# Kernel tuning notes

Measured on AMD Instinct MI355X. Metric: run time of the kernel, lower is better.

## Reference

```python
import jax, jax.numpy as jnp
import numpy as np


def _lstm_layer(x_sbi, w_ih, w_hh, b):
    """Custom LSTM layer with elu candidate/cell activations.
    x_sbi: [S, B, I]; w_ih: [4H, I]; w_hh: [4H, H]; b: [4H]. Gate order i,f,g,o.
    Returns outputs [S, B, H].
    """
    H = w_hh.shape[1]
    S, B, _ = x_sbi.shape
    # Precompute the input projection for all timesteps at once.
    xw = jnp.einsum('sbi,gi->sbg', x_sbi, w_ih) + b  # [S, B, 4H]

    def step(carry, xt):
        h, c = carry
        gates = xt + h @ w_hh.T  # [B, 4H]
        i = jax.nn.sigmoid(gates[:, 0 * H:1 * H])
        f = jax.nn.sigmoid(gates[:, 1 * H:2 * H])
        g = jax.nn.elu(gates[:, 2 * H:3 * H])      # custom cell activation
        o = jax.nn.sigmoid(gates[:, 3 * H:4 * H])
        c = f * c + i * g
        h = o * jax.nn.elu(c)                       # custom hidden activation
        return (h, c), h

    h0 = jnp.zeros((B, H), dtype=x_sbi.dtype)
    c0 = jnp.zeros((B, H), dtype=x_sbi.dtype)
    _, out = jax.lax.scan(step, (h0, c0), xw)
    return out  # [S, B, H]


def setup_inputs() -> dict:
    key = jax.random.key(0)
    ks = jax.random.split(key, 12)
    B, S, I, H = 256, 512, 64, 512
    s_in = 1.0 / np.sqrt(H)
    d = {
        'x': jax.random.normal(ks[0], (B, S, I), dtype=jnp.float32),
        'w_ih1': jax.random.normal(ks[1], (4 * H, I), dtype=jnp.float32) * s_in,
        'w_hh1': jax.random.normal(ks[2], (4 * H, H), dtype=jnp.float32) * s_in,
        'b1': jax.random.normal(ks[3], (4 * H,), dtype=jnp.float32) * s_in,
        'w_ih2': jax.random.normal(ks[4], (4 * H, H), dtype=jnp.float32) * s_in,
        'w_hh2': jax.random.normal(ks[5], (4 * H, H), dtype=jnp.float32) * s_in,
        'b2': jax.random.normal(ks[6], (4 * H,), dtype=jnp.float32) * s_in,
        'w_ih3': jax.random.normal(ks[7], (4 * H, H), dtype=jnp.float32) * s_in,
        'w_hh3': jax.random.normal(ks[8], (4 * H, H), dtype=jnp.float32) * s_in,
        'b3': jax.random.normal(ks[9], (4 * H,), dtype=jnp.float32) * s_in,
        'fc_w': jax.random.normal(ks[10], (1, H), dtype=jnp.float32) * s_in,
        'fc_b': jax.random.normal(ks[11], (1,), dtype=jnp.float32) * s_in,
    }
    return d


def reference(x, w_ih1, w_hh1, b1, w_ih2, w_hh2, b2, w_ih3, w_hh3, b3, fc_w, fc_b):
    # x: [B, S, I] -> seq-first [S, B, I] (matches torch permute(1,0,2))
    out = jnp.transpose(x, (1, 0, 2))
    out = _lstm_layer(out, w_ih1, w_hh1, b1)  # dropout = identity (eval)
    out = _lstm_layer(out, w_ih2, w_hh2, b2)
    out = _lstm_layer(out, w_ih3, w_hh3, b3)
    last = out[-1]                             # [B, H]
    return last @ fc_w.T + fc_b                # [B, 1]
```

## Files before the change

### kernel.cpp

```cpp
#include <hip/hip_runtime.h>
#include <stdint.h>
#include <stddef.h>

#define S_LEN 512
#define BATCH 256
#define NIN   64
#define HD    512
#define G4    2048
#define RING_D 32
#define BT    64

typedef _Float16 f16;
typedef _Float16 f16x8 __attribute__((ext_vector_type(8)));
typedef float    f32x4 __attribute__((ext_vector_type(4)));
typedef uint32_t u32x4 __attribute__((ext_vector_type(4)));
typedef uint64_t u64x2 __attribute__((ext_vector_type(2)));

__global__ void k_f32_to_f16(const float* __restrict__ src, f16* __restrict__ dst, int n) {
  int i = blockIdx.x * 256 + threadIdx.x;
  if (i < n) dst[i] = (f16)src[i];
}

__global__ void k_x_transpose(const float* __restrict__ x, f16* __restrict__ xin) {
  int idx = blockIdx.x * 256 + threadIdx.x;
  int i  = idx & 63;
  int sb = idx >> 6;
  int b  = sb & 255;
  int s  = sb >> 8;
  xin[idx] = (f16)x[((size_t)b * S_LEN + s) * NIN + i];
}

__global__ void k_zero_i32(uint32_t* p, int n) {
  int i = blockIdx.x * 256 + threadIdx.x;
  if (i < n) p[i] = 0u;
}

__global__ __launch_bounds__(512, 2) void k_fused(
    const f16* __restrict__ whh,
    const f16* __restrict__ wih,
    const float* __restrict__ b0,
    const float* __restrict__ b1,
    const float* __restrict__ b2,
    const f16* __restrict__ xin,
    f16* __restrict__ ring,
    int* __restrict__ flags,
    f16* __restrict__ hlast) {
  const int tid  = threadIdx.x;
  const int lane = tid & 63;
  const int wave = tid >> 6;
  const int l    = blockIdx.x >> 6;
  const int bi   = (blockIdx.x >> 4) & 3;
  const int gi   = blockIdx.x & 15;
  const int ln   = lane & 15;
  const int quad = lane >> 4;
  const int g    = wave >> 1;
  const int kh   = wave & 1;

  __shared__ __align__(16) char smem[131072];
  char*  lh_b  = smem;
  char*  lhp_b = smem + 65536;
  float* lg0   = (float*)smem;
  float* lg1   = (float*)(smem + 32768);

  auto swz = [](int row, int boff) { return row * 1024 + (boff ^ ((row & 7) << 4)); };

  const f16* whh_l = whh + (size_t)l * G4 * HD;
  const f16* wih_l = wih + (size_t)l * G4 * HD;
  const float* bias_l = (l == 0) ? b0 : (l == 1 ? b1 : b2);

  f16x8 wf[16][2];
  if (kh == 0 || l > 0) {
    const f16* W = kh ? wih_l : whh_l;
#pragma unroll
    for (int nb = 0; nb < 2; nb++) {
      const int r = g * 512 + gi * 32 + nb * 16 + ln;
#pragma unroll
      for (int ks = 0; ks < 16; ks++) {
        u32x4 tmp = *(const u32x4*)(W + (size_t)r * HD + ks * 32 + quad * 8);
        asm volatile("" : "+v"(tmp));
        wf[ks][nb] = __builtin_bit_cast(f16x8, tmp);
      }
    }
  } else {
#pragma unroll
    for (int nb = 0; nb < 2; nb++) {
      const int r = g * 512 + gi * 32 + nb * 16 + ln;
#pragma unroll
      for (int ks = 0; ks < 2; ks++) {
        u32x4 tmp = *(const u32x4*)(wih_l + (size_t)r * NIN + ks * 32 + quad * 8);
        asm volatile("" : "+v"(tmp));
        wf[ks][nb] = __builtin_bit_cast(f16x8, tmp);
      }
    }
  }

  const int brow = tid >> 5;
  const int hl_  = tid & 31;
  float cv[4] = {0.f, 0.f, 0.f, 0.f};
  const float bv0 = bias_l[0 * HD + gi * 32 + hl_];
  const float bv1 = bias_l[1 * HD + gi * 32 + hl_];
  const float bv2 = bias_l[2 * HD + gi * 32 + hl_];
  const float bv3 = bias_l[3 * HD + gi * 32 + hl_];

  int* fown = flags + l * 64 + bi * 16;
  int* myflag = fown + gi;
  const int* fprev = (l > 0) ? (flags + (l - 1) * 64 + bi * 16) : fown;
  const int* fnext = (l < 2) ? (flags + (l + 1) * 64 + bi * 16) : fown;

  for (int t = 0; t < S_LEN; t++) {
    {
      const int* fp = fown;
      int need = t;
      if (quad == 1 && l > 0)      { fp = fprev; need = t + 1; }
      else if (quad == 2 && l < 2) { fp = fnext; need = t + 2 - RING_D; }
      int v = __hip_atomic_load(fp + ln, __ATOMIC_RELAXED, __HIP_MEMORY_SCOPE_AGENT);
      while (!__all(v >= need)) {
        __builtin_amdgcn_s_sleep(1);
        v = __hip_atomic_load(fp + ln, __ATOMIC_RELAXED, __HIP_MEMORY_SCOPE_AGENT);
      }
    }
    asm volatile("" ::: "memory");

    const uint64_t* hown = (const uint64_t*)(ring
        + ((size_t)l * RING_D + (t & (RING_D - 1))) * (BATCH * HD)
        + (size_t)(bi * BT) * HD);
    uint64_t a0[8], a1[8];
#pragma unroll
    for (int j = 0; j < 8; j++) {
      a0[j] = __hip_atomic_load(hown + j * 1024 + tid * 2,     __ATOMIC_RELAXED, __HIP_MEMORY_SCOPE_AGENT);
      a1[j] = __hip_atomic_load(hown + j * 1024 + tid * 2 + 1, __ATOMIC_RELAXED, __HIP_MEMORY_SCOPE_AGENT);
    }
    if (l > 0) {
      const uint64_t* hprev = (const uint64_t*)(ring
          + ((size_t)(l - 1) * RING_D + ((t + 1) & (RING_D - 1))) * (BATCH * HD)
          + (size_t)(bi * BT) * HD);
      uint64_t p0[8], p1[8];
#pragma unroll
      for (int j = 0; j < 8; j++) {
        p0[j] = __hip_atomic_load(hprev + j * 1024 + tid * 2,     __ATOMIC_RELAXED, __HIP_MEMORY_SCOPE_AGENT);
        p1[j] = __hip_atomic_load(hprev + j * 1024 + tid * 2 + 1, __ATOMIC_RELAXED, __HIP_MEMORY_SCOPE_AGENT);
      }
#pragma unroll
      for (int j = 0; j < 8; j++) {
        const int e = j * 1024 + tid * 2, row = e >> 7, c8 = e & 127;
        u64x2 p; p[0] = p0[j]; p[1] = p1[j];
        *(u64x2*)(lhp_b + swz(row, c8 * 8)) = p;
      }
    } else {
      const int xr = tid >> 3, xc = tid & 7;
      u32x4 xv = *(const u32x4*)(xin + ((size_t)(t * 256 + bi * BT + xr)) * NIN + xc * 8);
      *(u32x4*)(lhp_b + swz(xr, xc * 16)) = xv;
    }
#pragma unroll
    for (int j = 0; j < 8; j++) {
      const int e = j * 1024 + tid * 2, row = e >> 7, c8 = e & 127;
      u64x2 p; p[0] = a0[j]; p[1] = a1[j];
      *(u64x2*)(lh_b + swz(row, c8 * 8)) = p;
    }
    __syncthreads();

    f32x4 acc[4][2] = {};
    const char* tb = kh ? lhp_b : lh_b;
    if (kh == 0 || l > 0) {
#pragma unroll
      for (int ks = 0; ks < 16; ks++) {
        f16x8 af[4];
#pragma unroll
        for (int mi = 0; mi < 4; mi++)
          af[mi] = *(const f16x8*)(tb + swz(mi * 16 + ln, ks * 64 + quad * 16));
#pragma unroll
        for (int mi = 0; mi < 4; mi++)
#pragma unroll
          for (int nb = 0; nb < 2; nb++)
            acc[mi][nb] = __builtin_amdgcn_mfma_f32_16x16x32_f16(af[mi], wf[ks][nb], acc[mi][nb], 0, 0, 0);
      }
    } else {
#pragma unroll
      for (int ks = 0; ks < 2; ks++) {
        f16x8 af[4];
#pragma unroll
        for (int mi = 0; mi < 4; mi++)
          af[mi] = *(const f16x8*)(tb + swz(mi * 16 + ln, ks * 64 + quad * 16));
#pragma unroll
        for (int mi = 0; mi < 4; mi++)
#pragma unroll
          for (int nb = 0; nb < 2; nb++)
            acc[mi][nb] = __builtin_amdgcn_mfma_f32_16x16x32_f16(af[mi], wf[ks][nb], acc[mi][nb], 0, 0, 0);
      }
    }
    __syncthreads();

    {
      float* lg = kh ? lg1 : lg0;
#pragma unroll
      for (int mi = 0; mi < 4; mi++)
#pragma unroll
        for (int nb = 0; nb < 2; nb++)
#pragma unroll
          for (int rr = 0; rr < 4; rr++) {
            const int row = mi * 16 + quad * 4 + rr;
            const int col = g * 32 + nb * 16 + ln;
            lg[row * 128 + (col ^ (((row >> 2) & 7) << 2))] = acc[mi][nb][rr];
          }
    }
    __syncthreads();

    f16* hout = ring + ((size_t)l * RING_D + ((t + 1) & (RING_D - 1))) * (BATCH * HD);
#pragma unroll
    for (int s = 0; s < 4; s++) {
      const int row = brow + s * 16;
      const int xm = ((row >> 2) & 7) << 2;
      const int rb = row * 128;
      float g0 = lg0[rb + ((0  + hl_) ^ xm)] + lg1[rb + ((0  + hl_) ^ xm)] + bv0;
      float g1 = lg0[rb + ((32 + hl_) ^ xm)] + lg1[rb + ((32 + hl_) ^ xm)] + bv1;
      float g2 = lg0[rb + ((64 + hl_) ^ xm)] + lg1[rb + ((64 + hl_) ^ xm)] + bv2;
      float g3 = lg0[rb + ((96 + hl_) ^ xm)] + lg1[rb + ((96 + hl_) ^ xm)] + bv3;
      const float igt = 1.f / (1.f + __expf(-g0));
      const float fgt = 1.f / (1.f + __expf(-g1));
      const float ggt = g2 > 0.f ? g2 : expm1f(g2);
      const float ogt = 1.f / (1.f + __expf(-g3));
      cv[s] = fgt * cv[s] + igt * ggt;
      const float hv = ogt * (cv[s] > 0.f ? cv[s] : expm1f(cv[s]));
      f16 hv16 = (f16)hv;
      unsigned short us;
      __builtin_memcpy(&us, &hv16, 2);
      const size_t col = (size_t)(bi * BT + row) * HD + gi * 32 + hl_;
      __hip_atomic_store((unsigned short*)(hout + col), us,
                         __ATOMIC_RELAXED, __HIP_MEMORY_SCOPE_AGENT);
      if (l == 2 && t == S_LEN - 1) hlast[col] = hv16;
    }
    __syncthreads();
    if (tid == 0)
      __hip_atomic_store(myflag, t + 1, __ATOMIC_RELAXED, __HIP_MEMORY_SCOPE_AGENT);
  }
}

__global__ __launch_bounds__(64) void k_fc(const f16* __restrict__ hlast,
                                           const float* __restrict__ fcw,
                                           const float* __restrict__ fcb,
                                           float* __restrict__ out) {
  const int b = blockIdx.x, lane = threadIdx.x;
  const f16* hp = hlast + (size_t)b * HD + lane * 8;
  float s = 0.f;
#pragma unroll
  for (int j = 0; j < 8; j++) s += (float)hp[j] * fcw[lane * 8 + j];
  for (int off = 32; off; off >>= 1) s += __shfl_down(s, off);
  if (lane == 0) out[b] = s + fcb[0];
}

extern "C" void kernel_launch(void* const* d_in, const int* in_sizes, int n_in,
                              void* d_out, int out_size, void* d_ws, size_t ws_size,
                              hipStream_t stream) {
  (void)in_sizes; (void)n_in; (void)out_size; (void)ws_size;
  const float* x      = (const float*)d_in[0];
  const float* wih[3] = {(const float*)d_in[1], (const float*)d_in[4], (const float*)d_in[7]};
  const float* whh[3] = {(const float*)d_in[2], (const float*)d_in[5], (const float*)d_in[8]};
  const float* bia[3] = {(const float*)d_in[3], (const float*)d_in[6], (const float*)d_in[9]};
  const float* fcw = (const float*)d_in[10];
  const float* fcb = (const float*)d_in[11];
  float* out = (float*)d_out;

  char* ws = (char*)d_ws;
  size_t off = 0;
  auto alloc = [&](size_t bytes) -> char* {
    off = (off + 255) & ~(size_t)255;
    char* p = ws + off;
    off += bytes;
    return p;
  };

  f16* xin   = (f16*)alloc((size_t)S_LEN * BATCH * NIN * 2);
  f16* wih16 = (f16*)alloc((size_t)3 * G4 * HD * 2);
  f16* whh16 = (f16*)alloc((size_t)3 * G4 * HD * 2);
  f16* ring  = (f16*)alloc((size_t)3 * RING_D * BATCH * HD * 2);
  int* flags = (int*)alloc(256 * 4);
  f16* hlast = (f16*)alloc((size_t)BATCH * HD * 2);

  {
    int n = S_LEN * BATCH * NIN;
    k_x_transpose<<<dim3(n / 256), dim3(256), 0, stream>>>(x, xin);
  }
  k_f32_to_f16<<<dim3((G4 * NIN + 255) / 256), dim3(256), 0, stream>>>(wih[0], wih16, G4 * NIN);
  k_f32_to_f16<<<dim3((G4 * HD + 255) / 256), dim3(256), 0, stream>>>(wih[1], wih16 + (size_t)G4 * HD, G4 * HD);
  k_f32_to_f16<<<dim3((G4 * HD + 255) / 256), dim3(256), 0, stream>>>(wih[2], wih16 + (size_t)2 * G4 * HD, G4 * HD);
  for (int l = 0; l < 3; l++)
    k_f32_to_f16<<<dim3((G4 * HD + 255) / 256), dim3(256), 0, stream>>>(whh[l], whh16 + (size_t)l * G4 * HD, G4 * HD);
  for (int l = 0; l < 3; l++)
    k_zero_i32<<<dim3(BATCH * HD / 2 / 256), dim3(256), 0, stream>>>(
        (uint32_t*)(ring + (size_t)l * RING_D * BATCH * HD), BATCH * HD / 2);
  k_zero_i32<<<dim3(1), dim3(256), 0, stream>>>((uint32_t*)flags, 192);

  k_fused<<<dim3(192), dim3(512), 0, stream>>>(whh16, wih16, bia[0], bia[1], bia[2],
                                               xin, ring, flags, hlast);

  k_fc<<<dim3(BATCH), dim3(64), 0, stream>>>(hlast, fcw, fcb, out);
}
```

Measured before the change: 5.788 ms.

## Overlap input-projection MFMA and next-step prefetch with recurrent h loads

Splits waves by role. The input-side waves (kh=1) compute the input/previous-layer projection into a shared gate buffer while the recurrent-side waves (kh=0) wait for and load h_{t-1}. Afterwards the kh=0 waves run the recurrent MFMA and accumulate into that buffer, while the kh=1 waves prefetch the next timestep's input (x or the lower layer's h). This takes the input projection and its loads off the critical recurrent path and replaces the double gate buffer with a single summed one. It also swaps expm1f for __expf-1, which is cheaper but loses some accuracy near zero, and raises LDS use to 160KB.

```diff
diff --git a/kernel.cpp b/kernel.cpp
--- a/kernel.cpp
+++ b/kernel.cpp
@@ -55,14 +55,15 @@
   const int quad = lane >> 4;
   const int g    = wave >> 1;
   const int kh   = wave & 1;
-
-  __shared__ __align__(16) char smem[131072];
+  const int gt   = (wave >> 1) * 64 + lane;
+
+  __shared__ __align__(16) char smem[163840];
   char*  lh_b  = smem;
   char*  lhp_b = smem + 65536;
-  float* lg0   = (float*)smem;
-  float* lg1   = (float*)(smem + 32768);
+  float* lgsum = (float*)(smem + 131072);
 
   auto swz = [](int row, int boff) { return row * 1024 + (boff ^ ((row & 7) << 4)); };
+  auto lgpos = [](int row, int col) { return row * 128 + (col ^ (((row >> 2) & 7) << 2)); };
 
   const f16* whh_l = whh + (size_t)l * G4 * HD;
   const f16* wih_l = wih + (size_t)l * G4 * HD;
@@ -107,91 +108,81 @@
   const int* fprev = (l > 0) ? (flags + (l - 1) * 64 + bi * 16) : fown;
   const int* fnext = (l < 2) ? (flags + (l + 1) * 64 + bi * 16) : fown;
 
-  for (int t = 0; t < S_LEN; t++) {
-    {
-      const int* fp = fown;
-      int need = t;
-      if (quad == 1 && l > 0)      { fp = fprev; need = t + 1; }
-      else if (quad == 2 && l < 2) { fp = fnext; need = t + 2 - RING_D; }
-      int v = __hip_atomic_load(fp + ln, __ATOMIC_RELAXED, __HIP_MEMORY_SCOPE_AGENT);
-      while (!__all(v >= need)) {
-        __builtin_amdgcn_s_sleep(1);
-        v = __hip_atomic_load(fp + ln, __ATOMIC_RELAXED, __HIP_MEMORY_SCOPE_AGENT);
-      }
+  if (l > 0) {
+    int v = __hip_atomic_load(fprev + ln, __ATOMIC_RELAXED, __HIP_MEMORY_SCOPE_AGENT);
+    while (!__all(v >= 1)) {
+      __builtin_amdgcn_s_sleep(1);
+      v = __hip_atomic_load(fprev + ln, __ATOMIC_RELAXED, __HIP_MEMORY_SCOPE_AGENT);
     }
     asm volatile("" ::: "memory");
-
-    const uint64_t* hown = (const uint64_t*)(ring
-        + ((size_t)l * RING_D + (t & (RING_D - 1))) * (BATCH * HD)
-        + (size_t)(bi * BT) * HD);
-    uint64_t a0[8], a1[8];
+    const uint64_t* hp = (const uint64_t*)(ring
+        + ((size_t)(l - 1) * RING_D + 1) * (BATCH * HD) + (size_t)(bi * BT) * HD);
+    uint64_t p0[8], p1[8];
 #pragma unroll
     for (int j = 0; j < 8; j++) {
-      a0[j] = __hip_atomic_load(hown + j * 1024 + tid * 2,     __ATOMIC_RELAXED, __HIP_MEMORY_SCOPE_AGENT);
-      a1[j] = __hip_atomic_load(hown + j * 1024 + tid * 2 + 1, __ATOMIC_RELAXED, __HIP_MEMORY_SCOPE_AGENT);
-    }
-    if (l > 0) {
-      const uint64_t* hprev = (const uint64_t*)(ring
-          + ((size_t)(l - 1) * RING_D + ((t + 1) & (RING_D - 1))) * (BATCH * HD)
-          + (size_t)(bi * BT) * HD);
-      uint64_t p0[8], p1[8];
-#pragma unroll
-      for (int j = 0; j < 8; j++) {
-        p0[j] = __hip_atomic_load(hprev + j * 1024 + tid * 2,     __ATOMIC_RELAXED, __HIP_MEMORY_SCOPE_AGENT);
-        p1[j] = __hip_atomic_load(hprev + j * 1024 + tid * 2 + 1, __ATOMIC_RELAXED, __HIP_MEMORY_SCOPE_AGENT);
-      }
-#pragma unroll
-      for (int j = 0; j < 8; j++) {
-        const int e = j * 1024 + tid * 2, row = e >> 7, c8 = e & 127;
-        u64x2 p; p[0] = p0[j]; p[1] = p1[j];
-        *(u64x2*)(lhp_b + swz(row, c8 * 8)) = p;
-      }
-    } else {
-      const int xr = tid >> 3, xc = tid & 7;
-      u32x4 xv = *(const u32x4*)(xin + ((size_t)(t * 256 + bi * BT + xr)) * NIN + xc * 8);
-      *(u32x4*)(lhp_b + swz(xr, xc * 16)) = xv;
+      p0[j] = __hip_atomic_load(hp + j * 1024 + tid * 2,     __ATOMIC_RELAXED, __HIP_MEMORY_SCOPE_AGENT);
+      p1[j] = __hip_atomic_load(hp + j * 1024 + tid * 2 + 1, __ATOMIC_RELAXED, __HIP_MEMORY_SCOPE_AGENT);
     }
 #pragma unroll
     for (int j = 0; j < 8; j++) {
       const int e = j * 1024 + tid * 2, row = e >> 7, c8 = e & 127;
-      u64x2 p; p[0] = a0[j]; p[1] = a1[j];
-      *(u64x2*)(lh_b + swz(row, c8 * 8)) = p;
-    }
-    __syncthreads();
-
-    f32x4 acc[4][2] = {};
-    const char* tb = kh ? lhp_b : lh_b;
-    if (kh == 0 || l > 0) {
-#pragma unroll
-      for (int ks = 0; ks < 16; ks++) {
+      u64x2 p; p[0] = p0[j]; p[1] = p1[j];
+      *(u64x2*)(lhp_b + swz(row, c8 * 8)) = p;
+    }
+  } else {
+    const int xr = tid >> 3, xc = tid & 7;
+    u32x4 xv = *(const u32x4*)(xin + ((size_t)(bi * BT + xr)) * NIN + xc * 8);
+    *(u32x4*)(lhp_b + swz(xr, xc * 16)) = xv;
+  }
+  __syncthreads();
+
+  for (int t = 0; t < S_LEN; t++) {
+    const bool lastT = (t == S_LEN - 1);
+
+    if (kh == 0) {
+      {
+        const int* fp = fown; int need = t;
+        if (quad == 2 && l < 2) { fp = fnext; need = t - 28; }
+        int v = __hip_atomic_load(fp + ln, __ATOMIC_RELAXED, __HIP_MEMORY_SCOPE_AGENT);
+        while (!__all(v >= need)) {
+          __builtin_amdgcn_s_sleep(1);
+          v = __hip_atomic_load(fp + ln, __ATOMIC_RELAXED, __HIP_MEMORY_SCOPE_AGENT);
+        }
+      }
+      asm volatile("" ::: "memory");
+      const uint64_t* hown = (const uint64_t*)(ring
+          + ((size_t)l * RING_D + (t & (RING_D - 1))) * (BATCH * HD)
+          + (size_t)(bi * BT) * HD);
+#pragma unroll
+      for (int b = 0; b < 2; b++) {
+        uint64_t q0[8], q1[8];
+#pragma unroll
+        for (int j = 0; j < 8; j++) {
+          const int e = (b * 8 + j) * 512 + gt * 2;
+          q0[j] = __hip_atomic_load(hown + e,     __ATOMIC_RELAXED, __HIP_MEMORY_SCOPE_AGENT);
+          q1[j] = __hip_atomic_load(hown + e + 1, __ATOMIC_RELAXED, __HIP_MEMORY_SCOPE_AGENT);
+        }
+#pragma unroll
+        for (int j = 0; j < 8; j++) {
+          const int e = (b * 8 + j) * 512 + gt * 2, row = e >> 7, c8 = e & 127;
+          u64x2 p; p[0] = q0[j]; p[1] = q1[j];
+          *(u64x2*)(lh_b + swz(row, c8 * 8)) = p;
+        }
+      }
+    } else {
+      f32x4 acc[4][2] = {};
+      const int nks = (l == 0) ? 2 : 16;
+      for (int ks = 0; ks < nks; ks++) {
         f16x8 af[4];
 #pragma unroll
         for (int mi = 0; mi < 4; mi++)
-          af[mi] = *(const f16x8*)(tb + swz(mi * 16 + ln, ks * 64 + quad * 16));
+          af[mi] = *(const f16x8*)(lhp_b + swz(mi * 16 + ln, ks * 64 + quad * 16));
 #pragma unroll
         for (int mi = 0; mi < 4; mi++)
 #pragma unroll
           for (int nb = 0; nb < 2; nb++)
             acc[mi][nb] = __builtin_amdgcn_mfma_f32_16x16x32_f16(af[mi], wf[ks][nb], acc[mi][nb], 0, 0, 0);
       }
-    } else {
-#pragma unroll
-      for (int ks = 0; ks < 2; ks++) {
-        f16x8 af[4];
-#pragma unroll
-        for (int mi = 0; mi < 4; mi++)
-          af[mi] = *(const f16x8*)(tb + swz(mi * 16 + ln, ks * 64 + quad * 16));
-#pragma unroll
-        for (int mi = 0; mi < 4; mi++)
-#pragma unroll
-          for (int nb = 0; nb < 2; nb++)
-            acc[mi][nb] = __builtin_amdgcn_mfma_f32_16x16x32_f16(af[mi], wf[ks][nb], acc[mi][nb], 0, 0, 0);
-      }
-    }
-    __syncthreads();
-
-    {
-      float* lg = kh ? lg1 : lg0;
 #pragma unroll
       for (int mi = 0; mi < 4; mi++)
 #pragma unroll
@@ -200,8 +191,70 @@
           for (int rr = 0; rr < 4; rr++) {
             const int row = mi * 16 + quad * 4 + rr;
             const int col = g * 32 + nb * 16 + ln;
-            lg[row * 128 + (col ^ (((row >> 2) & 7) << 2))] = acc[mi][nb][rr];
+            lgsum[lgpos(row, col)] = acc[mi][nb][rr];
           }
+    }
+    __syncthreads();
+
+    if (kh == 0) {
+      f32x4 acc[4][2] = {};
+#pragma unroll
+      for (int ks = 0; ks < 16; ks++) {
+        f16x8 af[4];
+#pragma unroll
+        for (int mi = 0; mi < 4; mi++)
+          af[mi] = *(const f16x8*)(lh_b + swz(mi * 16 + ln, ks * 64 + quad * 16));
+#pragma unroll
+        for (int mi = 0; mi < 4; mi++)
+#pragma unroll
+          for (int nb = 0; nb < 2; nb++)
+            acc[mi][nb] = __builtin_amdgcn_mfma_f32_16x16x32_f16(af[mi], wf[ks][nb], acc[mi][nb], 0, 0, 0);
+      }
+#pragma unroll
+      for (int mi = 0; mi < 4; mi++)
+#pragma unroll
+        for (int nb = 0; nb < 2; nb++)
+#pragma unroll
+          for (int rr = 0; rr < 4; rr++) {
+            const int row = mi * 16 + quad * 4 + rr;
+            const int col = g * 32 + nb * 16 + ln;
+            lgsum[lgpos(row, col)] += acc[mi][nb][rr];
+          }
+    } else if (!lastT) {
+      if (l > 0) {
+        int v = __hip_atomic_load(fprev + ln, __ATOMIC_RELAXED, __HIP_MEMORY_SCOPE_AGENT);
+        while (!__all(v >= t + 2)) {
+          __builtin_amdgcn_s_sleep(1);
+          v = __hip_atomic_load(fprev + ln, __ATOMIC_RELAXED, __HIP_MEMORY_SCOPE_AGENT);
+        }
+        asm volatile("" ::: "memory");
+        const uint64_t* hp = (const uint64_t*)(ring
+            + ((size_t)(l - 1) * RING_D + ((t + 2) & (RING_D - 1))) * (BATCH * HD)
+            + (size_t)(bi * BT) * HD);
+#pragma unroll
+        for (int b = 0; b < 2; b++) {
+          uint64_t q0[8], q1[8];
+#pragma unroll
+          for (int j = 0; j < 8; j++) {
+            const int e = (b * 8 + j) * 512 + gt * 2;
+            q0[j] = __hip_atomic_load(hp + e,     __ATOMIC_RELAXED, __HIP_MEMORY_SCOPE_AGENT);
+            q1[j] = __hip_atomic_load(hp + e + 1, __ATOMIC_RELAXED, __HIP_MEMORY_SCOPE_AGENT);
+          }
+#pragma unroll
+          for (int j = 0; j < 8; j++) {
+            const int e = (b * 8 + j) * 512 + gt * 2, row = e >> 7, c8 = e & 127;
+            u64x2 p; p[0] = q0[j]; p[1] = q1[j];
+            *(u64x2*)(lhp_b + swz(row, c8 * 8)) = p;
+          }
+        }
+      } else {
+#pragma unroll
+        for (int j = 0; j < 2; j++) {
+          const int cid = j * 256 + gt, xr = cid >> 3, xc = cid & 7;
+          u32x4 xv = *(const u32x4*)(xin + ((size_t)((t + 1) * 256 + bi * BT + xr)) * NIN + xc * 8);
+          *(u32x4*)(lhp_b + swz(xr, xc * 16)) = xv;
+        }
+      }
     }
     __syncthreads();
 
@@ -209,18 +262,16 @@
 #pragma unroll
     for (int s = 0; s < 4; s++) {
       const int row = brow + s * 16;
-      const int xm = ((row >> 2) & 7) << 2;
-      const int rb = row * 128;
-      float g0 = lg0[rb + ((0  + hl_) ^ xm)] + lg1[rb + ((0  + hl_) ^ xm)] + bv0;
-      float g1 = lg0[rb + ((32 + hl_) ^ xm)] + lg1[rb + ((32 + hl_) ^ xm)] + bv1;
-      float g2 = lg0[rb + ((64 + hl_) ^ xm)] + lg1[rb + ((64 + hl_) ^ xm)] + bv2;
-      float g3 = lg0[rb + ((96 + hl_) ^ xm)] + lg1[rb + ((96 + hl_) ^ xm)] + bv3;
+      float g0 = lgsum[lgpos(row, 0  + hl_)] + bv0;
+      float g1 = lgsum[lgpos(row, 32 + hl_)] + bv1;
+      float g2 = lgsum[lgpos(row, 64 + hl_)] + bv2;
+      float g3 = lgsum[lgpos(row, 96 + hl_)] + bv3;
       const float igt = 1.f / (1.f + __expf(-g0));
       const float fgt = 1.f / (1.f + __expf(-g1));
-      const float ggt = g2 > 0.f ? g2 : expm1f(g2);
+      const float ggt = g2 > 0.f ? g2 : (__expf(g2) - 1.f);
       const float ogt = 1.f / (1.f + __expf(-g3));
       cv[s] = fgt * cv[s] + igt * ggt;
-      const float hv = ogt * (cv[s] > 0.f ? cv[s] : expm1f(cv[s]));
+      const float hv = ogt * (cv[s] > 0.f ? cv[s] : (__expf(cv[s]) - 1.f));
       f16 hv16 = (f16)hv;
       unsigned short us;
       __builtin_memcpy(&us, &hv16, 2);
```

New measurement: 9.875 ms. 70.6% more time.

## Prefetch previous-layer input via direct global-to-LDS loads and overlap with gate math

Applied to the files above, without the earlier changes.

Replaces the register-staged atomic loads of the recurrent and previous-layer hidden states with global_load_lds DMA straight into swizzled LDS. The previous-layer or x input for step t+1 is now fetched at the end of step t, after the gate epilogue, so its latency is moved off the start of the next step. The loop also collapses the two MFMA branches into one with a variable trip count, swaps expm1f for __expf-1, and drops a full __syncthreads in favour of a raw s_barrier. This risks memory-ordering subtleties: plain DMA loads replace agent-scope atomics, the LDS slot reuse now relies on the waitcnt and barrier placement, and __expf-1 loses precision near zero.

```diff
diff --git a/kernel.cpp b/kernel.cpp
--- a/kernel.cpp
+++ b/kernel.cpp
@@ -14,7 +14,13 @@
 typedef _Float16 f16x8 __attribute__((ext_vector_type(8)));
 typedef float    f32x4 __attribute__((ext_vector_type(4)));
 typedef uint32_t u32x4 __attribute__((ext_vector_type(4)));
-typedef uint64_t u64x2 __attribute__((ext_vector_type(2)));
+
+typedef __attribute__((address_space(3))) void lds_as;
+typedef const __attribute__((address_space(1))) void glb_as;
+
+static __device__ __forceinline__ void gll16(const void* g, void* l) {
+  __builtin_amdgcn_global_load_lds((glb_as*)g, (lds_as*)l, 16, 0, 17);
+}
 
 __global__ void k_f32_to_f16(const float* __restrict__ src, f16* __restrict__ dst, int n) {
   int i = blockIdx.x * 256 + threadIdx.x;
@@ -63,6 +69,7 @@
   float* lg1   = (float*)(smem + 32768);
 
   auto swz = [](int row, int boff) { return row * 1024 + (boff ^ ((row & 7) << 4)); };
+  auto lgpos = [](int row, int col) { return row * 128 + (col ^ (((row >> 2) & 7) << 2)); };
 
   const f16* whh_l = whh + (size_t)l * G4 * HD;
   const f16* wih_l = wih + (size_t)l * G4 * HD;
@@ -107,12 +114,31 @@
   const int* fprev = (l > 0) ? (flags + (l - 1) * 64 + bi * 16) : fown;
   const int* fnext = (l < 2) ? (flags + (l + 1) * 64 + bi * 16) : fown;
 
+  if (l > 0) {
+    int v = __hip_atomic_load(fprev + ln, __ATOMIC_RELAXED, __HIP_MEMORY_SCOPE_AGENT);
+    while (!__all(v >= 1)) {
+      __builtin_amdgcn_s_sleep(1);
+      v = __hip_atomic_load(fprev + ln, __ATOMIC_RELAXED, __HIP_MEMORY_SCOPE_AGENT);
+    }
+    asm volatile("" ::: "memory");
+    const f16* src = ring + ((size_t)(l - 1) * RING_D + 1) * (BATCH * HD)
+                   + (size_t)(bi * BT) * HD;
+#pragma unroll
+    for (int jj = 0; jj < 8; jj++) {
+      const int r = wave * 8 + jj;
+      const int gb = (lane * 16) ^ ((r & 7) << 4);
+      gll16((const char*)(src + (size_t)r * HD) + gb, lhp_b + r * 1024);
+    }
+  } else {
+    const int xr = tid >> 3, xc = tid & 7;
+    u32x4 xv = *(const u32x4*)(xin + ((size_t)(bi * BT + xr)) * NIN + xc * 8);
+    *(u32x4*)(lhp_b + swz(xr, xc * 16)) = xv;
+  }
+
   for (int t = 0; t < S_LEN; t++) {
     {
-      const int* fp = fown;
-      int need = t;
-      if (quad == 1 && l > 0)      { fp = fprev; need = t + 1; }
-      else if (quad == 2 && l < 2) { fp = fnext; need = t + 2 - RING_D; }
+      const int* fp = fown; int need = t;
+      if (quad == 2 && l < 2) { fp = fnext; need = t - 28; }
       int v = __hip_atomic_load(fp + ln, __ATOMIC_RELAXED, __HIP_MEMORY_SCOPE_AGENT);
       while (!__all(v >= need)) {
         __builtin_amdgcn_s_sleep(1);
@@ -121,72 +147,36 @@
     }
     asm volatile("" ::: "memory");
 
-    const uint64_t* hown = (const uint64_t*)(ring
-        + ((size_t)l * RING_D + (t & (RING_D - 1))) * (BATCH * HD)
-        + (size_t)(bi * BT) * HD);
-    uint64_t a0[8], a1[8];
-#pragma unroll
-    for (int j = 0; j < 8; j++) {
-      a0[j] = __hip_atomic_load(hown + j * 1024 + tid * 2,     __ATOMIC_RELAXED, __HIP_MEMORY_SCOPE_AGENT);
-      a1[j] = __hip_atomic_load(hown + j * 1024 + tid * 2 + 1, __ATOMIC_RELAXED, __HIP_MEMORY_SCOPE_AGENT);
-    }
-    if (l > 0) {
-      const uint64_t* hprev = (const uint64_t*)(ring
-          + ((size_t)(l - 1) * RING_D + ((t + 1) & (RING_D - 1))) * (BATCH * HD)
-          + (size_t)(bi * BT) * HD);
-      uint64_t p0[8], p1[8];
-#pragma unroll
-      for (int j = 0; j < 8; j++) {
-        p0[j] = __hip_atomic_load(hprev + j * 1024 + tid * 2,     __ATOMIC_RELAXED, __HIP_MEMORY_SCOPE_AGENT);
-        p1[j] = __hip_atomic_load(hprev + j * 1024 + tid * 2 + 1, __ATOMIC_RELAXED, __HIP_MEMORY_SCOPE_AGENT);
-      }
-#pragma unroll
-      for (int j = 0; j < 8; j++) {
-        const int e = j * 1024 + tid * 2, row = e >> 7, c8 = e & 127;
-        u64x2 p; p[0] = p0[j]; p[1] = p1[j];
-        *(u64x2*)(lhp_b + swz(row, c8 * 8)) = p;
-      }
-    } else {
+    {
+      const f16* src = ring + ((size_t)l * RING_D + (t & (RING_D - 1))) * (BATCH * HD)
+                     + (size_t)(bi * BT) * HD;
+#pragma unroll
+      for (int jj = 0; jj < 8; jj++) {
+        const int r = wave * 8 + jj;
+        const int gb = (lane * 16) ^ ((r & 7) << 4);
+        gll16((const char*)(src + (size_t)r * HD) + gb, lh_b + r * 1024);
+      }
+    }
+    u32x4 xv = {};
+    if (l == 0 && t + 1 < S_LEN) {
       const int xr = tid >> 3, xc = tid & 7;
-      u32x4 xv = *(const u32x4*)(xin + ((size_t)(t * 256 + bi * BT + xr)) * NIN + xc * 8);
-      *(u32x4*)(lhp_b + swz(xr, xc * 16)) = xv;
-    }
-#pragma unroll
-    for (int j = 0; j < 8; j++) {
-      const int e = j * 1024 + tid * 2, row = e >> 7, c8 = e & 127;
-      u64x2 p; p[0] = a0[j]; p[1] = a1[j];
-      *(u64x2*)(lh_b + swz(row, c8 * 8)) = p;
+      xv = *(const u32x4*)(xin + ((size_t)((t + 1) * 256 + bi * BT + xr)) * NIN + xc * 8);
     }
     __syncthreads();
 
     f32x4 acc[4][2] = {};
     const char* tb = kh ? lhp_b : lh_b;
-    if (kh == 0 || l > 0) {
-#pragma unroll
-      for (int ks = 0; ks < 16; ks++) {
-        f16x8 af[4];
-#pragma unroll
-        for (int mi = 0; mi < 4; mi++)
-          af[mi] = *(const f16x8*)(tb + swz(mi * 16 + ln, ks * 64 + quad * 16));
-#pragma unroll
-        for (int mi = 0; mi < 4; mi++)
-#pragma unroll
-          for (int nb = 0; nb < 2; nb++)
-            acc[mi][nb] = __builtin_amdgcn_mfma_f32_16x16x32_f16(af[mi], wf[ks][nb], acc[mi][nb], 0, 0, 0);
-      }
-    } else {
-#pragma unroll
-      for (int ks = 0; ks < 2; ks++) {
-        f16x8 af[4];
-#pragma unroll
-        for (int mi = 0; mi < 4; mi++)
-          af[mi] = *(const f16x8*)(tb + swz(mi * 16 + ln, ks * 64 + quad * 16));
-#pragma unroll
-        for (int mi = 0; mi < 4; mi++)
-#pragma unroll
-          for (int nb = 0; nb < 2; nb++)
-            acc[mi][nb] = __builtin_amdgcn_mfma_f32_16x16x32_f16(af[mi], wf[ks][nb], acc[mi][nb], 0, 0, 0);
-      }
+    const int nks = (kh && l == 0) ? 2 : 16;
+    for (int ks = 0; ks < nks; ks++) {
+      f16x8 af[4];
+#pragma unroll
+      for (int mi = 0; mi < 4; mi++)
+        af[mi] = *(const f16x8*)(tb + swz(mi * 16 + ln, ks * 64 + quad * 16));
+#pragma unroll
+      for (int mi = 0; mi < 4; mi++)
+#pragma unroll
+        for (int nb = 0; nb < 2; nb++)
+          acc[mi][nb] = __builtin_amdgcn_mfma_f32_16x16x32_f16(af[mi], wf[ks][nb], acc[mi][nb], 0, 0, 0);
     }
     __syncthreads();
 
@@ -217,10 +207,10 @@
       float g3 = lg0[rb + ((96 + hl_) ^ xm)] + lg1[rb + ((96 + hl_) ^ xm)] + bv3;
       const float igt = 1.f / (1.f + __expf(-g0));
       const float fgt = 1.f / (1.f + __expf(-g1));
-      const float ggt = g2 > 0.f ? g2 : expm1f(g2);
+      const float ggt = g2 > 0.f ? g2 : (__expf(g2) - 1.f);
       const float ogt = 1.f / (1.f + __expf(-g3));
       cv[s] = fgt * cv[s] + igt * ggt;
-      const float hv = ogt * (cv[s] > 0.f ? cv[s] : expm1f(cv[s]));
+      const float hv = ogt * (cv[s] > 0.f ? cv[s] : (__expf(cv[s]) - 1.f));
       f16 hv16 = (f16)hv;
       unsigned short us;
       __builtin_memcpy(&us, &hv16, 2);
@@ -229,7 +219,33 @@
                          __ATOMIC_RELAXED, __HIP_MEMORY_SCOPE_AGENT);
       if (l == 2 && t == S_LEN - 1) hlast[col] = hv16;
     }
-    __syncthreads();
+
+    asm volatile("s_waitcnt vmcnt(0)" ::: "memory");
+
+    if (t + 1 < S_LEN) {
+      if (l > 0) {
+        int v = __hip_atomic_load(fprev + ln, __ATOMIC_RELAXED, __HIP_MEMORY_SCOPE_AGENT);
+        while (!__all(v >= t + 2)) {
+          __builtin_amdgcn_s_sleep(1);
+          v = __hip_atomic_load(fprev + ln, __ATOMIC_RELAXED, __HIP_MEMORY_SCOPE_AGENT);
+        }
+        asm volatile("" ::: "memory");
+        const f16* src = ring + ((size_t)(l - 1) * RING_D + ((t + 2) & (RING_D - 1))) * (BATCH * HD)
+                       + (size_t)(bi * BT) * HD;
+#pragma unroll
+        for (int jj = 0; jj < 8; jj++) {
+          const int r = wave * 8 + jj;
+          const int gb = (lane * 16) ^ ((r & 7) << 4);
+          gll16((const char*)(src + (size_t)r * HD) + gb, lhp_b + r * 1024);
+        }
+      } else {
+        const int xr = tid >> 3, xc = tid & 7;
+        *(u32x4*)(lhp_b + swz(xr, xc * 16)) = xv;
+      }
+    }
+
+    __builtin_amdgcn_s_barrier();
+    __builtin_amdgcn_sched_barrier(0);
     if (tid == 0)
       __hip_atomic_store(myflag, t + 1, __ATOMIC_RELAXED, __HIP_MEMORY_SCOPE_AGENT);
   }
```

New measurement: 7.721 ms. 33.4% more time.

## Map LSTM blocks to XCDs and read same-XCD recurrent state through L2 with direct LDS loads

Applied to the files above, without the earlier changes.

Blocks are remapped so that layers 0-1 of each batch slice share one XCD and layer 2 sits on its own XCD. At startup each block records its hardware XCC id and checks whether its producers share it. When they do, the hidden state is read from a second, non-atomic ring copy using global_load_lds straight into LDS, so the L2 is used instead of device-scope atomic loads. The ring depth also shrinks from 32 to 8, and expm1f is replaced by __expf-1. In exchange every step writes two copies of the state, the launch adds 64 idle blocks, and coherence between the two ring copies rests on the assumed XCD placement.

```diff
diff --git a/kernel.cpp b/kernel.cpp
--- a/kernel.cpp
+++ b/kernel.cpp
@@ -7,7 +7,7 @@
 #define NIN   64
 #define HD    512
 #define G4    2048
-#define RING_D 32
+#define RING_D 8
 #define BT    64
 
 typedef _Float16 f16;
@@ -15,6 +15,13 @@
 typedef float    f32x4 __attribute__((ext_vector_type(4)));
 typedef uint32_t u32x4 __attribute__((ext_vector_type(4)));
 typedef uint64_t u64x2 __attribute__((ext_vector_type(2)));
+
+typedef __attribute__((address_space(3))) void lds_as;
+typedef const __attribute__((address_space(1))) void glb_as;
+
+static __device__ __forceinline__ void gll16_l2(const void* g, void* l) {
+  __builtin_amdgcn_global_load_lds((glb_as*)g, (lds_as*)l, 16, 0, 1);
+}
 
 __global__ void k_f32_to_f16(const float* __restrict__ src, f16* __restrict__ dst, int n) {
   int i = blockIdx.x * 256 + threadIdx.x;
@@ -42,15 +49,19 @@
     const float* __restrict__ b1,
     const float* __restrict__ b2,
     const f16* __restrict__ xin,
-    f16* __restrict__ ring,
+    f16* __restrict__ ringM,
+    f16* __restrict__ ringL,
     int* __restrict__ flags,
+    int* __restrict__ xcdmap,
     f16* __restrict__ hlast) {
   const int tid  = threadIdx.x;
   const int lane = tid & 63;
   const int wave = tid >> 6;
-  const int l    = blockIdx.x >> 6;
-  const int bi   = (blockIdx.x >> 4) & 3;
-  const int gi   = blockIdx.x & 15;
+  const int xcd  = blockIdx.x & 7;
+  const int slot = blockIdx.x >> 3;
+  int l, bi, gi;
+  if (xcd < 4) { bi = xcd; l = slot >> 4; gi = slot & 15; }
+  else         { if (slot >= 16) return; l = 2; bi = xcd - 4; gi = slot; }
   const int ln   = lane & 15;
   const int quad = lane >> 4;
   const int g    = wave >> 1;
@@ -63,10 +74,37 @@
   float* lg1   = (float*)(smem + 32768);
 
   auto swz = [](int row, int boff) { return row * 1024 + (boff ^ ((row & 7) << 4)); };
+  auto bid_of = [](int ll, int bb, int gg) {
+    return (ll == 2) ? ((gg << 3) | (bb + 4)) : ((((ll << 4) + gg) << 3) | bb);
+  };
 
   const f16* whh_l = whh + (size_t)l * G4 * HD;
   const f16* wih_l = wih + (size_t)l * G4 * HD;
   const float* bias_l = (l == 0) ? b0 : (l == 1 ? b1 : b2);
+
+  unsigned myxcc;
+  asm volatile("s_getreg_b32 %0, hwreg(HW_REG_XCC_ID)" : "=s"(myxcc));
+  if (tid == 0)
+    __hip_atomic_store(xcdmap + blockIdx.x, (int)myxcc + 1, __ATOMIC_RELAXED, __HIP_MEMORY_SCOPE_AGENT);
+  bool lh_local = false, lhp_local = false;
+  {
+    const int mb = bid_of(l, bi, ln);
+    int v = __hip_atomic_load(xcdmap + mb, __ATOMIC_RELAXED, __HIP_MEMORY_SCOPE_AGENT);
+    while (!__all(v > 0)) {
+      __builtin_amdgcn_s_sleep(2);
+      v = __hip_atomic_load(xcdmap + mb, __ATOMIC_RELAXED, __HIP_MEMORY_SCOPE_AGENT);
+    }
+    lh_local = __all(v == (int)myxcc + 1);
+  }
+  if (l == 1) {
+    const int pb = bid_of(0, bi, ln);
+    int v = __hip_atomic_load(xcdmap + pb, __ATOMIC_RELAXED, __HIP_MEMORY_SCOPE_AGENT);
+    while (!__all(v > 0)) {
+      __builtin_amdgcn_s_sleep(2);
+      v = __hip_atomic_load(xcdmap + pb, __ATOMIC_RELAXED, __HIP_MEMORY_SCOPE_AGENT);
+    }
+    lhp_local = __all(v == (int)myxcc + 1);
+  }
 
   f16x8 wf[16][2];
   if (kh == 0 || l > 0) {
@@ -121,17 +159,48 @@
     }
     asm volatile("" ::: "memory");
 
-    const uint64_t* hown = (const uint64_t*)(ring
-        + ((size_t)l * RING_D + (t & (RING_D - 1))) * (BATCH * HD)
-        + (size_t)(bi * BT) * HD);
-    uint64_t a0[8], a1[8];
-#pragma unroll
-    for (int j = 0; j < 8; j++) {
-      a0[j] = __hip_atomic_load(hown + j * 1024 + tid * 2,     __ATOMIC_RELAXED, __HIP_MEMORY_SCOPE_AGENT);
-      a1[j] = __hip_atomic_load(hown + j * 1024 + tid * 2 + 1, __ATOMIC_RELAXED, __HIP_MEMORY_SCOPE_AGENT);
-    }
-    if (l > 0) {
-      const uint64_t* hprev = (const uint64_t*)(ring
+    if (lh_local) {
+      const f16* src = ringL + ((size_t)l * RING_D + (t & (RING_D - 1))) * (BATCH * HD)
+                     + (size_t)(bi * BT) * HD;
+#pragma unroll
+      for (int jj = 0; jj < 8; jj++) {
+        const int r = wave * 8 + jj;
+        const int gb = (lane * 16) ^ ((r & 7) << 4);
+        gll16_l2((const char*)(src + (size_t)r * HD) + gb, lh_b + r * 1024);
+      }
+    } else {
+      const uint64_t* hown = (const uint64_t*)(ringM
+          + ((size_t)l * RING_D + (t & (RING_D - 1))) * (BATCH * HD)
+          + (size_t)(bi * BT) * HD);
+      uint64_t a0[8], a1[8];
+#pragma unroll
+      for (int j = 0; j < 8; j++) {
+        a0[j] = __hip_atomic_load(hown + j * 1024 + tid * 2,     __ATOMIC_RELAXED, __HIP_MEMORY_SCOPE_AGENT);
+        a1[j] = __hip_atomic_load(hown + j * 1024 + tid * 2 + 1, __ATOMIC_RELAXED, __HIP_MEMORY_SCOPE_AGENT);
+      }
+#pragma unroll
+      for (int j = 0; j < 8; j++) {
+        const int e = j * 1024 + tid * 2, row = e >> 7, c8 = e & 127;
+        u64x2 p; p[0] = a0[j]; p[1] = a1[j];
+        *(u64x2*)(lh_b + swz(row, c8 * 8)) = p;
+      }
+    }
+
+    if (l == 0) {
+      const int xr = tid >> 3, xc = tid & 7;
+      u32x4 xv = *(const u32x4*)(xin + ((size_t)(t * 256 + bi * BT + xr)) * NIN + xc * 8);
+      *(u32x4*)(lhp_b + swz(xr, xc * 16)) = xv;
+    } else if (l == 1 && lhp_local) {
+      const f16* src = ringL + ((size_t)0 * RING_D + ((t + 1) & (RING_D - 1))) * (BATCH * HD)
+                     + (size_t)(bi * BT) * HD;
+#pragma unroll
+      for (int jj = 0; jj < 8; jj++) {
+        const int r = wave * 8 + jj;
+        const int gb = (lane * 16) ^ ((r & 7) << 4);
+        gll16_l2((const char*)(src + (size_t)r * HD) + gb, lhp_b + r * 1024);
+      }
+    } else {
+      const uint64_t* hprev = (const uint64_t*)(ringM
           + ((size_t)(l - 1) * RING_D + ((t + 1) & (RING_D - 1))) * (BATCH * HD)
           + (size_t)(bi * BT) * HD);
       uint64_t p0[8], p1[8];
@@ -146,47 +215,22 @@
         u64x2 p; p[0] = p0[j]; p[1] = p1[j];
         *(u64x2*)(lhp_b + swz(row, c8 * 8)) = p;
       }
-    } else {
-      const int xr = tid >> 3, xc = tid & 7;
-      u32x4 xv = *(const u32x4*)(xin + ((size_t)(t * 256 + bi * BT + xr)) * NIN + xc * 8);
-      *(u32x4*)(lhp_b + swz(xr, xc * 16)) = xv;
-    }
-#pragma unroll
-    for (int j = 0; j < 8; j++) {
-      const int e = j * 1024 + tid * 2, row = e >> 7, c8 = e & 127;
-      u64x2 p; p[0] = a0[j]; p[1] = a1[j];
-      *(u64x2*)(lh_b + swz(row, c8 * 8)) = p;
     }
     __syncthreads();
 
     f32x4 acc[4][2] = {};
     const char* tb = kh ? lhp_b : lh_b;
-    if (kh == 0 || l > 0) {
-#pragma unroll
-      for (int ks = 0; ks < 16; ks++) {
-        f16x8 af[4];
-#pragma unroll
-        for (int mi = 0; mi < 4; mi++)
-          af[mi] = *(const f16x8*)(tb + swz(mi * 16 + ln, ks * 64 + quad * 16));
-#pragma unroll
-        for (int mi = 0; mi < 4; mi++)
-#pragma unroll
-          for (int nb = 0; nb < 2; nb++)
-            acc[mi][nb] = __builtin_amdgcn_mfma_f32_16x16x32_f16(af[mi], wf[ks][nb], acc[mi][nb], 0, 0, 0);
-      }
-    } else {
-#pragma unroll
-      for (int ks = 0; ks < 2; ks++) {
-        f16x8 af[4];
-#pragma unroll
-        for (int mi = 0; mi < 4; mi++)
-          af[mi] = *(const f16x8*)(tb + swz(mi * 16 + ln, ks * 64 + quad * 16));
-#pragma unroll
-        for (int mi = 0; mi < 4; mi++)
-#pragma unroll
-          for (int nb = 0; nb < 2; nb++)
-            acc[mi][nb] = __builtin_amdgcn_mfma_f32_16x16x32_f16(af[mi], wf[ks][nb], acc[mi][nb], 0, 0, 0);
-      }
+    const int nks = (kh && l == 0) ? 2 : 16;
+    for (int ks = 0; ks < nks; ks++) {
+      f16x8 af[4];
+#pragma unroll
+      for (int mi = 0; mi < 4; mi++)
+        af[mi] = *(const f16x8*)(tb + swz(mi * 16 + ln, ks * 64 + quad * 16));
+#pragma unroll
+      for (int mi = 0; mi < 4; mi++)
+#pragma unroll
+        for (int nb = 0; nb < 2; nb++)
+          acc[mi][nb] = __builtin_amdgcn_mfma_f32_16x16x32_f16(af[mi], wf[ks][nb], acc[mi][nb], 0, 0, 0);
     }
     __syncthreads();
 
@@ -205,7 +249,9 @@
     }
     __syncthreads();
 
-    f16* hout = ring + ((size_t)l * RING_D + ((t + 1) & (RING_D - 1))) * (BATCH * HD);
+    const size_t slotoff = ((size_t)l * RING_D + ((t + 1) & (RING_D - 1))) * (BATCH * HD);
+    f16* houtM = ringM + slotoff;
+    f16* houtL = ringL + slotoff;
 #pragma unroll
     for (int s = 0; s < 4; s++) {
       const int row = brow + s * 16;
@@ -217,15 +263,16 @@
       float g3 = lg0[rb + ((96 + hl_) ^ xm)] + lg1[rb + ((96 + hl_) ^ xm)] + bv3;
       const float igt = 1.f / (1.f + __expf(-g0));
       const float fgt = 1.f / (1.f + __expf(-g1));
-      const float ggt = g2 > 0.f ? g2 : expm1f(g2);
+      const float ggt = g2 > 0.f ? g2 : (__expf(g2) - 1.f);
       const float ogt = 1.f / (1.f + __expf(-g3));
       cv[s] = fgt * cv[s] + igt * ggt;
-      const float hv = ogt * (cv[s] > 0.f ? cv[s] : expm1f(cv[s]));
+      const float hv = ogt * (cv[s] > 0.f ? cv[s] : (__expf(cv[s]) - 1.f));
       f16 hv16 = (f16)hv;
       unsigned short us;
       __builtin_memcpy(&us, &hv16, 2);
       const size_t col = (size_t)(bi * BT + row) * HD + gi * 32 + hl_;
-      __hip_atomic_store((unsigned short*)(hout + col), us,
+      houtL[col] = hv16;
+      __hip_atomic_store((unsigned short*)(houtM + col), us,
                          __ATOMIC_RELAXED, __HIP_MEMORY_SCOPE_AGENT);
       if (l == 2 && t == S_LEN - 1) hlast[col] = hv16;
     }
@@ -272,8 +319,10 @@
   f16* xin   = (f16*)alloc((size_t)S_LEN * BATCH * NIN * 2);
   f16* wih16 = (f16*)alloc((size_t)3 * G4 * HD * 2);
   f16* whh16 = (f16*)alloc((size_t)3 * G4 * HD * 2);
-  f16* ring  = (f16*)alloc((size_t)3 * RING_D * BATCH * HD * 2);
+  f16* ringM = (f16*)alloc((size_t)3 * RING_D * BATCH * HD * 2);
+  f16* ringL = (f16*)alloc((size_t)3 * RING_D * BATCH * HD * 2);
   int* flags = (int*)alloc(256 * 4);
+  int* xcdmap= (int*)alloc(256 * 4);
   f16* hlast = (f16*)alloc((size_t)BATCH * HD * 2);
 
   {
@@ -285,13 +334,17 @@
   k_f32_to_f16<<<dim3((G4 * HD + 255) / 256), dim3(256), 0, stream>>>(wih[2], wih16 + (size_t)2 * G4 * HD, G4 * HD);
   for (int l = 0; l < 3; l++)
     k_f32_to_f16<<<dim3((G4 * HD + 255) / 256), dim3(256), 0, stream>>>(whh[l], whh16 + (size_t)l * G4 * HD, G4 * HD);
-  for (int l = 0; l < 3; l++)
+  for (int l = 0; l < 3; l++) {
     k_zero_i32<<<dim3(BATCH * HD / 2 / 256), dim3(256), 0, stream>>>(
-        (uint32_t*)(ring + (size_t)l * RING_D * BATCH * HD), BATCH * HD / 2);
+        (uint32_t*)(ringM + (size_t)l * RING_D * BATCH * HD), BATCH * HD / 2);
+    k_zero_i32<<<dim3(BATCH * HD / 2 / 256), dim3(256), 0, stream>>>(
+        (uint32_t*)(ringL + (size_t)l * RING_D * BATCH * HD), BATCH * HD / 2);
+  }
   k_zero_i32<<<dim3(1), dim3(256), 0, stream>>>((uint32_t*)flags, 192);
-
-  k_fused<<<dim3(192), dim3(512), 0, stream>>>(whh16, wih16, bia[0], bia[1], bia[2],
-                                               xin, ring, flags, hlast);
+  k_zero_i32<<<dim3(1), dim3(256), 0, stream>>>((uint32_t*)xcdmap, 256);
+
+  k_fused<<<dim3(256), dim3(512), 0, stream>>>(whh16, wih16, bia[0], bia[1], bia[2],
+                                               xin, ringM, ringL, flags, xcdmap, hlast);
 
   k_fc<<<dim3(BATCH), dim3(64), 0, stream>>>(hlast, fcw, fcb, out);
 }
```

New measurement: 7.043 ms. 1.22x slower.
